# Performance work log

Measured on AMD Instinct MI355X. Metric: run time of the kernel, lower is better.

The kernel has to match this reference:

```python
import jax, jax.numpy as jnp
import numpy as np

B = 2048        # graphs per batch
NC = 81         # cells per sudoku
IN_C, HID = 10, 128
N_ACT, N_NUM, N_TECH = 4, 9, 10


def _sudoku_edges():
    idx = np.arange(NC).reshape(9, 9)
    adj = np.zeros((NC, NC), dtype=bool)
    for i in range(9):
        for j in range(9):
            n = idx[i, j]
            adj[n, idx[i, :]] = True
            adj[n, idx[:, j]] = True
            bi, bj = 3 * (i // 3), 3 * (j // 3)
            adj[n, idx[bi:bi + 3, bj:bj + 3].reshape(-1)] = True
            adj[n, n] = False
    src, dst = np.nonzero(adj)  # 1620 directed edges
    return np.stack([src, dst]).astype(np.int32)


def setup_inputs() -> dict:
    key = jax.random.key(0)
    ks = jax.random.split(key, 12)
    N = B * NC
    base = _sudoku_edges()                          # [2, 1620]
    offs = (np.arange(B, dtype=np.int32) * NC)      # [B]
    ei = (base[:, None, :] + offs[None, :, None]).reshape(2, -1)  # [2, B*1620]
    batch = np.repeat(np.arange(B, dtype=np.int32), NC)           # [N]

    def lin(k, fan_in, fan_out):
        s = 1.0 / np.sqrt(fan_in)
        return jax.random.uniform(k, (fan_in, fan_out), jnp.float32, -s, s)

    return {
        "x": jax.random.normal(ks[0], (N, IN_C), jnp.float32),
        "edge_index": jnp.asarray(ei),
        "batch": jnp.asarray(batch),
        "W1": lin(ks[1], IN_C, HID), "b1": jnp.zeros((HID,), jnp.float32),
        "W2": lin(ks[2], HID, HID),  "b2": jnp.zeros((HID,), jnp.float32),
        "Wa": lin(ks[3], HID, N_ACT),  "ba": jnp.zeros((N_ACT,), jnp.float32),
        "Wc": lin(ks[4], HID, NC),     "bc": jnp.zeros((NC,), jnp.float32),
        "Wn": lin(ks[5], HID, N_NUM),  "bn": jnp.zeros((N_NUM,), jnp.float32),
        "Wt": lin(ks[6], HID, N_TECH), "bt": jnp.zeros((N_TECH,), jnp.float32),
    }


def _gcn_conv(x, edge_index, W, b):
    n = x.shape[0]
    loop = jnp.arange(n, dtype=edge_index.dtype)
    src = jnp.concatenate([edge_index[0], loop])
    dst = jnp.concatenate([edge_index[1], loop])
    deg = jax.ops.segment_sum(jnp.ones_like(dst, jnp.float32), dst, num_segments=n)
    dinv = jax.lax.rsqrt(deg)            # deg >= 1 due to self-loops
    norm = dinv[src] * dinv[dst]         # [E+N]
    h = x @ W                            # [N, out]
    msg = h[src] * norm[:, None]         # gather + scale
    return jax.ops.segment_sum(msg, dst, num_segments=n) + b


def reference(x, edge_index, batch, W1, b1, W2, b2, Wa, ba, Wc, bc, Wn, bn, Wt, bt):
    h = jax.nn.relu(_gcn_conv(x, edge_index, W1, b1))
    h = jax.nn.relu(_gcn_conv(h, edge_index, W2, b2))
    # global mean pool over graphs
    sums = jax.ops.segment_sum(h, batch, num_segments=B)
    cnts = jax.ops.segment_sum(jnp.ones((h.shape[0],), h.dtype), batch, num_segments=B)
    pooled = sums / jnp.maximum(cnts, 1.0)[:, None]   # [B, HID]
    return (pooled @ Wa + ba, pooled @ Wc + bc, pooled @ Wn + bn, pooled @ Wt + bt)
```

## Files before the change

kernel.cpp:

```cpp
#include <hip/hip_runtime.h>
#include <hip/hip_bf16.h>

typedef __attribute__((ext_vector_type(8))) short bf16x8;
typedef __attribute__((ext_vector_type(4))) float f32x4;

__device__ __forceinline__ unsigned short f2b(float f) {
    __hip_bfloat16 h = __float2bfloat16(f);
    return __builtin_bit_cast(unsigned short, h);
}
__device__ __forceinline__ float b2f(unsigned short u) {
    unsigned v = ((unsigned)u) << 16;
    return __builtin_bit_cast(float, v);
}
__device__ __forceinline__ float ldf(const void* p, int idx, bool f32) {
    return f32 ? ((const float*)p)[idx] : b2f(((const unsigned short*)p)[idx]);
}
__device__ __forceinline__ unsigned short ldb(const void* p, int idx, bool f32) {
    return f32 ? f2b(((const float*)p)[idx]) : ((const unsigned short*)p)[idx];
}

__device__ __forceinline__ bool sniff_f32(const void* x) {
    const unsigned* p = (const unsigned*)x;
    int wild = 0;
#pragma unroll
    for (int i = 0; i < 16; ++i) {
        unsigned e = (p[i] >> 7) & 0xFF;
        wild += (e != 0 && (e < 0x68 || e > 0x90)) ? 1 : 0;
    }
    return wild > 8;
}

#define WS_B1F    16
#define WS_B2F    528
#define WS_BHF    1040
#define WS_W1R    1536
#define WS_W2R    9728
#define WS_SR     42496
#define WS_WH     60928

__global__ void k_repack(const void* __restrict__ x,
                         const void* __restrict__ W1, const void* __restrict__ b1,
                         const void* __restrict__ W2, const void* __restrict__ b2,
                         const void* __restrict__ Wa, const void* __restrict__ ba,
                         const void* __restrict__ Wc, const void* __restrict__ bc,
                         const void* __restrict__ Wn, const void* __restrict__ bn,
                         const void* __restrict__ Wt, const void* __restrict__ bt,
                         char* __restrict__ ws) {
    const bool f32 = sniff_f32(x);
    int idx = blockIdx.x * blockDim.x + threadIdx.x;
    if (idx < 4096) {
        int f = idx >> 5, k = idx & 31;
        unsigned short v = (k < 10) ? ldb(W1, k * 128 + f, f32) : (unsigned short)0;
        ((unsigned short*)(ws + WS_W1R))[idx] = v;
        return;
    }
    idx -= 4096;
    if (idx < 16384) {
        int f = idx >> 7, k = idx & 127;
        ((unsigned short*)(ws + WS_W2R))[idx] = ldb(W2, k * 128 + f, f32);
        return;
    }
    idx -= 16384;
    if (idx < 9216) {
        int fi = idx >> 9, rem = idx & 511;
        int lane = rem >> 3, j = rem & 7;
        int mi = fi / 3, kc = fi - mi * 3;
        int node = mi * 16 + (lane & 15);
        int cell = kc * 32 + ((lane >> 4) << 3) + j;
        bool adj = false;
        if (node < 81 && cell < 81) {
            int ni = node / 9, nj = node % 9;
            int ci = cell / 9, cj = cell % 9;
            adj = (ni == ci) || (nj == cj) ||
                  ((ni / 3 == ci / 3) && (nj / 3 == cj / 3));
        }
        ((unsigned short*)(ws + WS_SR))[idx] = adj ? (unsigned short)0x3F80 : (unsigned short)0;
        return;
    }
    idx -= 9216;
    if (idx < 13312) {
        int o = idx >> 7, f = idx & 127;
        const void* W; int oo, dim;
        if (o < 4)       { W = Wa; oo = o;      dim = 4;  }
        else if (o < 85) { W = Wc; oo = o - 4;  dim = 81; }
        else if (o < 94) { W = Wn; oo = o - 85; dim = 9;  }
        else             { W = Wt; oo = o - 94; dim = 10; }
        ((float*)(ws + WS_WH))[idx] = ldf(W, f * dim + oo, f32);
        return;
    }
    idx -= 13312;
    if (idx < 360) {
        float v;
        if (idx < 128)      v = ldf(b1, idx, f32);
        else if (idx < 256) v = ldf(b2, idx - 128, f32);
        else {
            int o = idx - 256;
            if (o < 4)       v = ldf(ba, o, f32);
            else if (o < 85) v = ldf(bc, o - 4, f32);
            else if (o < 94) v = ldf(bn, o - 85, f32);
            else             v = ldf(bt, o - 94, f32);
        }
        if (idx < 128)      ((float*)(ws + WS_B1F))[idx] = v;
        else if (idx < 256) ((float*)(ws + WS_B2F))[idx - 128] = v;
        else                ((float*)(ws + WS_BHF))[idx - 256] = v;
    }
}

#define T_STRIDE 104
#define H_STRIDE 136

__global__ __launch_bounds__(256, 4) void sudoku_gnn(
    const void* __restrict__ x, const char* __restrict__ ws,
    void* __restrict__ out, int nB)
{
    __shared__ __attribute__((aligned(16))) unsigned short sBuf[13312];
    __shared__ __attribute__((aligned(16))) unsigned int   xs[816];
    __shared__ float sPoolPart[256];
    __shared__ float sPool[128];

    const bool f32 = sniff_f32(x);
    const unsigned short* w1r = (const unsigned short*)(ws + WS_W1R);
    const unsigned short* w2r = (const unsigned short*)(ws + WS_W2R);
    const unsigned short* sr  = (const unsigned short*)(ws + WS_SR);
    const float* b1f = (const float*)(ws + WS_B1F);
    const float* b2f = (const float*)(ws + WS_B2F);
    const float* bhf = (const float*)(ws + WS_BHF);
    const float* whf = (const float*)(ws + WS_WH);

    const int tid  = threadIdx.x;
    const int wave = tid >> 6;
    const int lane = tid & 63;
    const int ln15 = lane & 15;
    const int q    = lane >> 4;
    const int k0   = q * 8;
    const int mtb  = (wave & 1) * 3;
    const int nb   = (wave & 1) * 48;
    const int fb   = (wave >> 1) * 64;
    const int g    = blockIdx.x;
    const float inv21 = 1.0f / 21.0f;

    {
        const int words = f32 ? 810 : 405;
        const unsigned int* src = (const unsigned int*)x + (size_t)g * words;
        for (int i = tid; i < words; i += 256) xs[i] = src[i];
    }

    bf16x8 sfr[3][3];
#pragma unroll
    for (int kc = 0; kc < 3; ++kc)
#pragma unroll
        for (int jt = 0; jt < 3; ++jt)
            sfr[kc][jt] = *(const bf16x8*)&sr[(((mtb + jt) * 3 + kc) * 64 + lane) * 8];
    bf16x8 w1f[4];
#pragma unroll
    for (int nt = 0; nt < 4; ++nt)
        w1f[nt] = *(const bf16x8*)&w1r[(fb + nt * 16 + ln15) * 32 + k0];

    __syncthreads();

    bf16x8 xf[3];
#pragma unroll
    for (int mt = 0; mt < 3; ++mt) {
        int node = (mtb + mt) * 16 + ln15;
        bf16x8 v = {0, 0, 0, 0, 0, 0, 0, 0};
        if (node < 81) {
            if (q == 0) {
#pragma unroll
                for (int jj = 0; jj < 8; ++jj)
                    v[jj] = (short)(f32 ? f2b(((const float*)xs)[node * 10 + jj])
                                        : ((const unsigned short*)xs)[node * 10 + jj]);
            } else if (q == 1) {
#pragma unroll
                for (int jj = 0; jj < 2; ++jj)
                    v[jj] = (short)(f32 ? f2b(((const float*)xs)[node * 10 + 8 + jj])
                                        : ((const unsigned short*)xs)[node * 10 + 8 + jj]);
            }
        }
        xf[mt] = v;
    }

    const f32x4 z4 = {0.f, 0.f, 0.f, 0.f};
    f32x4 acc[3][4];

#pragma unroll
    for (int mt = 0; mt < 3; ++mt)
#pragma unroll
        for (int nt = 0; nt < 4; ++nt)
            acc[mt][nt] = __builtin_amdgcn_mfma_f32_16x16x32_bf16(xf[mt], w1f[nt], z4, 0, 0, 0);
#pragma unroll
    for (int mt = 0; mt < 3; ++mt)
#pragma unroll
        for (int nt = 0; nt < 4; ++nt) {
            int f = fb + nt * 16 + ln15;
            int nodeb = (mtb + mt) * 16 + q * 4;
            unsigned lo = (unsigned)f2b(acc[mt][nt][0]) | ((unsigned)f2b(acc[mt][nt][1]) << 16);
            unsigned hi = (unsigned)f2b(acc[mt][nt][2]) | ((unsigned)f2b(acc[mt][nt][3]) << 16);
            *(uint2*)&sBuf[f * T_STRIDE + nodeb] = make_uint2(lo, hi);
        }
    __syncthreads();

#pragma unroll
    for (int at = 0; at < 3; ++at)
#pragma unroll
        for (int jt = 0; jt < 4; ++jt) acc[at][jt] = z4;
#pragma unroll
    for (int kc = 0; kc < 3; ++kc) {
        bf16x8 a4[4];
#pragma unroll
        for (int at = 0; at < 4; ++at)
            a4[at] = *(const bf16x8*)&sBuf[(fb + at * 16 + ln15) * T_STRIDE + kc * 32 + k0];
#pragma unroll
        for (int at = 0; at < 4; ++at)
#pragma unroll
            for (int jt = 0; jt < 3; ++jt)
                acc[jt][at] = __builtin_amdgcn_mfma_f32_16x16x32_bf16(a4[at], sfr[kc][jt], acc[jt][at], 0, 0, 0);
    }
    __syncthreads();
#pragma unroll
    for (int at = 0; at < 4; ++at) {
        float4 bv = *(const float4*)&b1f[fb + at * 16 + q * 4];
#pragma unroll
        for (int jt = 0; jt < 3; ++jt) {
            int node = nb + jt * 16 + ln15;
            float v0 = fmaxf(acc[jt][at][0] * inv21 + bv.x, 0.0f);
            float v1 = fmaxf(acc[jt][at][1] * inv21 + bv.y, 0.0f);
            float v2 = fmaxf(acc[jt][at][2] * inv21 + bv.z, 0.0f);
            float v3 = fmaxf(acc[jt][at][3] * inv21 + bv.w, 0.0f);
            unsigned lo = (unsigned)f2b(v0) | ((unsigned)f2b(v1) << 16);
            unsigned hi = (unsigned)f2b(v2) | ((unsigned)f2b(v3) << 16);
            *(uint2*)&sBuf[node * H_STRIDE + fb + at * 16 + q * 4] = make_uint2(lo, hi);
        }
    }
    __syncthreads();

#pragma unroll
    for (int mt = 0; mt < 3; ++mt)
#pragma unroll
        for (int nt = 0; nt < 4; ++nt) acc[mt][nt] = z4;
#pragma unroll
    for (int kc = 0; kc < 4; ++kc) {
        bf16x8 w2f[4];
#pragma unroll
        for (int nt = 0; nt < 4; ++nt)
            w2f[nt] = *(const bf16x8*)&w2r[(fb + nt * 16 + ln15) * 128 + kc * 32 + k0];
        bf16x8 a3[3];
#pragma unroll
        for (int mt = 0; mt < 3; ++mt)
            a3[mt] = *(const bf16x8*)&sBuf[((mtb + mt) * 16 + ln15) * H_STRIDE + kc * 32 + k0];
#pragma unroll
        for (int mt = 0; mt < 3; ++mt)
#pragma unroll
            for (int nt = 0; nt < 4; ++nt)
                acc[mt][nt] = __builtin_amdgcn_mfma_f32_16x16x32_bf16(a3[mt], w2f[nt], acc[mt][nt], 0, 0, 0);
    }
    __syncthreads();
#pragma unroll
    for (int mt = 0; mt < 3; ++mt)
#pragma unroll
        for (int nt = 0; nt < 4; ++nt) {
            int f = fb + nt * 16 + ln15;
            int nodeb = (mtb + mt) * 16 + q * 4;
            unsigned lo = (unsigned)f2b(acc[mt][nt][0]) | ((unsigned)f2b(acc[mt][nt][1]) << 16);
            unsigned hi = (unsigned)f2b(acc[mt][nt][2]) | ((unsigned)f2b(acc[mt][nt][3]) << 16);
            *(uint2*)&sBuf[f * T_STRIDE + nodeb] = make_uint2(lo, hi);
        }
    __syncthreads();

#pragma unroll
    for (int at = 0; at < 3; ++at)
#pragma unroll
        for (int jt = 0; jt < 4; ++jt) acc[at][jt] = z4;
#pragma unroll
    for (int kc = 0; kc < 3; ++kc) {
        bf16x8 a4[4];
#pragma unroll
        for (int at = 0; at < 4; ++at)
            a4[at] = *(const bf16x8*)&sBuf[(fb + at * 16 + ln15) * T_STRIDE + kc * 32 + k0];
#pragma unroll
        for (int at = 0; at < 4; ++at)
#pragma unroll
            for (int jt = 0; jt < 3; ++jt)
                acc[jt][at] = __builtin_amdgcn_mfma_f32_16x16x32_bf16(a4[at], sfr[kc][jt], acc[jt][at], 0, 0, 0);
    }
#pragma unroll
    for (int at = 0; at < 4; ++at) {
        float4 bv = *(const float4*)&b2f[fb + at * 16 + q * 4];
        float s0 = 0.f, s1 = 0.f, s2 = 0.f, s3 = 0.f;
#pragma unroll
        for (int jt = 0; jt < 3; ++jt) {
            int node = nb + jt * 16 + ln15;
            if (node < 81) {
                s0 += fmaxf(acc[jt][at][0] * inv21 + bv.x, 0.0f);
                s1 += fmaxf(acc[jt][at][1] * inv21 + bv.y, 0.0f);
                s2 += fmaxf(acc[jt][at][2] * inv21 + bv.z, 0.0f);
                s3 += fmaxf(acc[jt][at][3] * inv21 + bv.w, 0.0f);
            }
        }
#pragma unroll
        for (int off = 1; off < 16; off <<= 1) {
            s0 += __shfl_xor(s0, off);
            s1 += __shfl_xor(s1, off);
            s2 += __shfl_xor(s2, off);
            s3 += __shfl_xor(s3, off);
        }
        if (ln15 == 0) {
            float4 v = {s0, s1, s2, s3};
            *(float4*)&sPoolPart[(wave & 1) * 128 + fb + at * 16 + q * 4] = v;
        }
    }
    __syncthreads();
    if (tid < 128) sPool[tid] = (sPoolPart[tid] + sPoolPart[128 + tid]) / 81.0f;
    __syncthreads();

    if (tid < 104) {
        float a = bhf[tid];
        const float4* wrow = (const float4*)(whf + tid * 128);
        const float4* sp4  = (const float4*)sPool;
#pragma unroll 8
        for (int i = 0; i < 32; ++i) {
            float4 wv = wrow[i];
            float4 pv = sp4[i];
            a += pv.x * wv.x + pv.y * wv.y + pv.z * wv.z + pv.w * wv.w;
        }
        int o = tid, oo; size_t off;
        if (o < 4)       { oo = o;      off = (size_t)g * 4 + oo; }
        else if (o < 85) { oo = o - 4;  off = (size_t)nB * 4  + (size_t)g * 81 + oo; }
        else if (o < 94) { oo = o - 85; off = (size_t)nB * 85 + (size_t)g * 9  + oo; }
        else             { oo = o - 94; off = (size_t)nB * 94 + (size_t)g * 10 + oo; }
        if (f32) ((float*)out)[off] = a;
        else     ((unsigned short*)out)[off] = f2b(a);
    }
}

extern "C" void kernel_launch(void* const* d_in, const int* in_sizes, int n_in,
                              void* d_out, int out_size, void* d_ws, size_t ws_size,
                              hipStream_t stream) {
    const void* x  = d_in[0];
    int nB = in_sizes[2] / 81;
    if (nB <= 0) return;

    char* ws = (char*)d_ws;
    hipLaunchKernelGGL(k_repack, dim3(170), dim3(256), 0, stream,
                       x, d_in[3], d_in[4], d_in[5], d_in[6],
                       d_in[7], d_in[8], d_in[9], d_in[10],
                       d_in[11], d_in[12], d_in[13], d_in[14], ws);
    hipLaunchKernelGGL(sudoku_gnn, dim3(nB), dim3(256), 0, stream,
                       x, (const char*)ws, d_out, nB);
}
```

Before: 147.6 us.

## Process two sudoku graphs per block with XOR-swizzled LDS layout

Each workgroup now handles two graphs, so per-block setup (sniffing the input, loading the structure and W1 fragments, loading W2 per k-chunk) is shared across twice the work, and the two graphs interleave their MFMA chains. The padded-stride shared buffers are replaced by two 128-wide buffers with an XOR swizzle to avoid bank conflicts. In exchange register pressure roughly doubles (launch bounds lowered to 2 blocks/CU), LDS use grows, and the grid halves to 1024 blocks, which may reduce latency hiding on a 256-CU device.

```diff
diff --git a/kernel.cpp b/kernel.cpp
--- a/kernel.cpp
+++ b/kernel.cpp
@@ -17,6 +17,9 @@
 }
 __device__ __forceinline__ unsigned short ldb(const void* p, int idx, bool f32) {
     return f32 ? f2b(((const float*)p)[idx]) : ((const unsigned short*)p)[idx];
+}
+__device__ __forceinline__ int swz(int row, int col) {
+    return row * 128 + (((col >> 3) ^ (row & 7)) << 3) + (col & 7);
 }
 
 __device__ __forceinline__ bool sniff_f32(const void* x) {
@@ -106,17 +109,15 @@
     }
 }
 
-#define T_STRIDE 104
-#define H_STRIDE 136
-
-__global__ __launch_bounds__(256, 4) void sudoku_gnn(
+__global__ __launch_bounds__(256, 2) void sudoku_gnn(
     const void* __restrict__ x, const char* __restrict__ ws,
     void* __restrict__ out, int nB)
 {
-    __shared__ __attribute__((aligned(16))) unsigned short sBuf[13312];
-    __shared__ __attribute__((aligned(16))) unsigned int   xs[816];
-    __shared__ float sPoolPart[256];
-    __shared__ float sPool[128];
+    __shared__ __attribute__((aligned(16))) unsigned short sA[16384];
+    __shared__ __attribute__((aligned(16))) unsigned short sB[16384];
+    __shared__ __attribute__((aligned(16))) unsigned int   xs2[1632];
+    __shared__ float sPoolPart[2][256];
+    __shared__ float sPool[2][128];
 
     const bool f32 = sniff_f32(x);
     const unsigned short* w1r = (const unsigned short*)(ws + WS_W1R);
@@ -136,13 +137,17 @@
     const int mtb  = (wave & 1) * 3;
     const int nb   = (wave & 1) * 48;
     const int fb   = (wave >> 1) * 64;
-    const int g    = blockIdx.x;
+    const int g0   = blockIdx.x * 2;
+    const int g1   = g0 + 1;
+    const bool hasB = (g1 < nB);
     const float inv21 = 1.0f / 21.0f;
+    unsigned short* const buf[2] = {sA, sB};
 
     {
         const int words = f32 ? 810 : 405;
-        const unsigned int* src = (const unsigned int*)x + (size_t)g * words;
-        for (int i = tid; i < words; i += 256) xs[i] = src[i];
+        const int tot = words * (hasB ? 2 : 1);
+        const unsigned int* src = (const unsigned int*)x + (size_t)g0 * words;
+        for (int i = tid; i < tot; i += 256) xs2[i] = src[i];
     }
 
     bf16x8 sfr[3][3];
@@ -158,177 +163,217 @@
 
     __syncthreads();
 
-    bf16x8 xf[3];
-#pragma unroll
-    for (int mt = 0; mt < 3; ++mt) {
-        int node = (mtb + mt) * 16 + ln15;
-        bf16x8 v = {0, 0, 0, 0, 0, 0, 0, 0};
-        if (node < 81) {
-            if (q == 0) {
-#pragma unroll
-                for (int jj = 0; jj < 8; ++jj)
-                    v[jj] = (short)(f32 ? f2b(((const float*)xs)[node * 10 + jj])
-                                        : ((const unsigned short*)xs)[node * 10 + jj]);
-            } else if (q == 1) {
-#pragma unroll
-                for (int jj = 0; jj < 2; ++jj)
-                    v[jj] = (short)(f32 ? f2b(((const float*)xs)[node * 10 + 8 + jj])
-                                        : ((const unsigned short*)xs)[node * 10 + 8 + jj]);
-            }
-        }
-        xf[mt] = v;
-    }
+    bf16x8 xf[2][3];
+#pragma unroll
+    for (int gg = 0; gg < 2; ++gg)
+#pragma unroll
+        for (int mt = 0; mt < 3; ++mt) {
+            int node = (mtb + mt) * 16 + ln15;
+            bf16x8 v = {0, 0, 0, 0, 0, 0, 0, 0};
+            if (node < 81) {
+                int base = gg * 810 + node * 10;
+                if (q == 0) {
+#pragma unroll
+                    for (int jj = 0; jj < 8; ++jj)
+                        v[jj] = (short)(f32 ? f2b(((const float*)xs2)[base + jj])
+                                            : ((const unsigned short*)xs2)[base + jj]);
+                } else if (q == 1) {
+#pragma unroll
+                    for (int jj = 0; jj < 2; ++jj)
+                        v[jj] = (short)(f32 ? f2b(((const float*)xs2)[base + 8 + jj])
+                                            : ((const unsigned short*)xs2)[base + 8 + jj]);
+                }
+            }
+            xf[gg][mt] = v;
+        }
 
     const f32x4 z4 = {0.f, 0.f, 0.f, 0.f};
-    f32x4 acc[3][4];
-
-#pragma unroll
-    for (int mt = 0; mt < 3; ++mt)
-#pragma unroll
-        for (int nt = 0; nt < 4; ++nt)
-            acc[mt][nt] = __builtin_amdgcn_mfma_f32_16x16x32_bf16(xf[mt], w1f[nt], z4, 0, 0, 0);
-#pragma unroll
-    for (int mt = 0; mt < 3; ++mt)
-#pragma unroll
-        for (int nt = 0; nt < 4; ++nt) {
-            int f = fb + nt * 16 + ln15;
-            int nodeb = (mtb + mt) * 16 + q * 4;
-            unsigned lo = (unsigned)f2b(acc[mt][nt][0]) | ((unsigned)f2b(acc[mt][nt][1]) << 16);
-            unsigned hi = (unsigned)f2b(acc[mt][nt][2]) | ((unsigned)f2b(acc[mt][nt][3]) << 16);
-            *(uint2*)&sBuf[f * T_STRIDE + nodeb] = make_uint2(lo, hi);
-        }
-    __syncthreads();
-
-#pragma unroll
-    for (int at = 0; at < 3; ++at)
-#pragma unroll
-        for (int jt = 0; jt < 4; ++jt) acc[at][jt] = z4;
+    f32x4 acc[2][3][4];
+
+#pragma unroll
+    for (int gg = 0; gg < 2; ++gg)
+#pragma unroll
+        for (int mt = 0; mt < 3; ++mt)
+#pragma unroll
+            for (int nt = 0; nt < 4; ++nt)
+                acc[gg][mt][nt] = __builtin_amdgcn_mfma_f32_16x16x32_bf16(xf[gg][mt], w1f[nt], z4, 0, 0, 0);
+#pragma unroll
+    for (int gg = 0; gg < 2; ++gg)
+#pragma unroll
+        for (int mt = 0; mt < 3; ++mt)
+#pragma unroll
+            for (int nt = 0; nt < 4; ++nt) {
+                int f = fb + nt * 16 + ln15;
+                int nodeb = (mtb + mt) * 16 + q * 4;
+                unsigned lo = (unsigned)f2b(acc[gg][mt][nt][0]) | ((unsigned)f2b(acc[gg][mt][nt][1]) << 16);
+                unsigned hi = (unsigned)f2b(acc[gg][mt][nt][2]) | ((unsigned)f2b(acc[gg][mt][nt][3]) << 16);
+                *(uint2*)&buf[gg][swz(f, nodeb)] = make_uint2(lo, hi);
+            }
+    __syncthreads();
+
+#pragma unroll
+    for (int gg = 0; gg < 2; ++gg)
+#pragma unroll
+        for (int a = 0; a < 3; ++a)
+#pragma unroll
+            for (int b = 0; b < 4; ++b) acc[gg][a][b] = z4;
 #pragma unroll
     for (int kc = 0; kc < 3; ++kc) {
-        bf16x8 a4[4];
-#pragma unroll
-        for (int at = 0; at < 4; ++at)
-            a4[at] = *(const bf16x8*)&sBuf[(fb + at * 16 + ln15) * T_STRIDE + kc * 32 + k0];
-#pragma unroll
-        for (int at = 0; at < 4; ++at)
-#pragma unroll
-            for (int jt = 0; jt < 3; ++jt)
-                acc[jt][at] = __builtin_amdgcn_mfma_f32_16x16x32_bf16(a4[at], sfr[kc][jt], acc[jt][at], 0, 0, 0);
-    }
-    __syncthreads();
-#pragma unroll
-    for (int at = 0; at < 4; ++at) {
-        float4 bv = *(const float4*)&b1f[fb + at * 16 + q * 4];
-#pragma unroll
-        for (int jt = 0; jt < 3; ++jt) {
-            int node = nb + jt * 16 + ln15;
-            float v0 = fmaxf(acc[jt][at][0] * inv21 + bv.x, 0.0f);
-            float v1 = fmaxf(acc[jt][at][1] * inv21 + bv.y, 0.0f);
-            float v2 = fmaxf(acc[jt][at][2] * inv21 + bv.z, 0.0f);
-            float v3 = fmaxf(acc[jt][at][3] * inv21 + bv.w, 0.0f);
-            unsigned lo = (unsigned)f2b(v0) | ((unsigned)f2b(v1) << 16);
-            unsigned hi = (unsigned)f2b(v2) | ((unsigned)f2b(v3) << 16);
-            *(uint2*)&sBuf[node * H_STRIDE + fb + at * 16 + q * 4] = make_uint2(lo, hi);
-        }
-    }
-    __syncthreads();
-
-#pragma unroll
-    for (int mt = 0; mt < 3; ++mt)
-#pragma unroll
-        for (int nt = 0; nt < 4; ++nt) acc[mt][nt] = z4;
+        bf16x8 a4[2][4];
+#pragma unroll
+        for (int gg = 0; gg < 2; ++gg)
+#pragma unroll
+            for (int at = 0; at < 4; ++at)
+                a4[gg][at] = *(const bf16x8*)&buf[gg][swz(fb + at * 16 + ln15, kc * 32 + k0)];
+#pragma unroll
+        for (int gg = 0; gg < 2; ++gg)
+#pragma unroll
+            for (int at = 0; at < 4; ++at)
+#pragma unroll
+                for (int jt = 0; jt < 3; ++jt)
+                    acc[gg][jt][at] = __builtin_amdgcn_mfma_f32_16x16x32_bf16(a4[gg][at], sfr[kc][jt], acc[gg][jt][at], 0, 0, 0);
+    }
+    __syncthreads();
+#pragma unroll
+    for (int gg = 0; gg < 2; ++gg)
+#pragma unroll
+        for (int at = 0; at < 4; ++at) {
+            float4 bv = *(const float4*)&b1f[fb + at * 16 + q * 4];
+#pragma unroll
+            for (int jt = 0; jt < 3; ++jt) {
+                int node = nb + jt * 16 + ln15;
+                float v0 = fmaxf(acc[gg][jt][at][0] * inv21 + bv.x, 0.0f);
+                float v1 = fmaxf(acc[gg][jt][at][1] * inv21 + bv.y, 0.0f);
+                float v2 = fmaxf(acc[gg][jt][at][2] * inv21 + bv.z, 0.0f);
+                float v3 = fmaxf(acc[gg][jt][at][3] * inv21 + bv.w, 0.0f);
+                unsigned lo = (unsigned)f2b(v0) | ((unsigned)f2b(v1) << 16);
+                unsigned hi = (unsigned)f2b(v2) | ((unsigned)f2b(v3) << 16);
+                *(uint2*)&buf[gg][swz(node, fb + at * 16 + q * 4)] = make_uint2(lo, hi);
+            }
+        }
+    __syncthreads();
+
+#pragma unroll
+    for (int gg = 0; gg < 2; ++gg)
+#pragma unroll
+        for (int a = 0; a < 3; ++a)
+#pragma unroll
+            for (int b = 0; b < 4; ++b) acc[gg][a][b] = z4;
 #pragma unroll
     for (int kc = 0; kc < 4; ++kc) {
         bf16x8 w2f[4];
 #pragma unroll
         for (int nt = 0; nt < 4; ++nt)
             w2f[nt] = *(const bf16x8*)&w2r[(fb + nt * 16 + ln15) * 128 + kc * 32 + k0];
-        bf16x8 a3[3];
+        bf16x8 a3[2][3];
+#pragma unroll
+        for (int gg = 0; gg < 2; ++gg)
+#pragma unroll
+            for (int mt = 0; mt < 3; ++mt)
+                a3[gg][mt] = *(const bf16x8*)&buf[gg][swz((mtb + mt) * 16 + ln15, kc * 32 + k0)];
+#pragma unroll
+        for (int gg = 0; gg < 2; ++gg)
+#pragma unroll
+            for (int mt = 0; mt < 3; ++mt)
+#pragma unroll
+                for (int nt = 0; nt < 4; ++nt)
+                    acc[gg][mt][nt] = __builtin_amdgcn_mfma_f32_16x16x32_bf16(a3[gg][mt], w2f[nt], acc[gg][mt][nt], 0, 0, 0);
+    }
+    __syncthreads();
+#pragma unroll
+    for (int gg = 0; gg < 2; ++gg)
 #pragma unroll
         for (int mt = 0; mt < 3; ++mt)
-            a3[mt] = *(const bf16x8*)&sBuf[((mtb + mt) * 16 + ln15) * H_STRIDE + kc * 32 + k0];
-#pragma unroll
-        for (int mt = 0; mt < 3; ++mt)
-#pragma unroll
-            for (int nt = 0; nt < 4; ++nt)
-                acc[mt][nt] = __builtin_amdgcn_mfma_f32_16x16x32_bf16(a3[mt], w2f[nt], acc[mt][nt], 0, 0, 0);
-    }
-    __syncthreads();
-#pragma unroll
-    for (int mt = 0; mt < 3; ++mt)
-#pragma unroll
-        for (int nt = 0; nt < 4; ++nt) {
-            int f = fb + nt * 16 + ln15;
-            int nodeb = (mtb + mt) * 16 + q * 4;
-            unsigned lo = (unsigned)f2b(acc[mt][nt][0]) | ((unsigned)f2b(acc[mt][nt][1]) << 16);
-            unsigned hi = (unsigned)f2b(acc[mt][nt][2]) | ((unsigned)f2b(acc[mt][nt][3]) << 16);
-            *(uint2*)&sBuf[f * T_STRIDE + nodeb] = make_uint2(lo, hi);
-        }
-    __syncthreads();
-
-#pragma unroll
-    for (int at = 0; at < 3; ++at)
-#pragma unroll
-        for (int jt = 0; jt < 4; ++jt) acc[at][jt] = z4;
+#pragma unroll
+            for (int nt = 0; nt < 4; ++nt) {
+                int f = fb + nt * 16 + ln15;
+                int nodeb = (mtb + mt) * 16 + q * 4;
+                unsigned lo = (unsigned)f2b(acc[gg][mt][nt][0]) | ((unsigned)f2b(acc[gg][mt][nt][1]) << 16);
+                unsigned hi = (unsigned)f2b(acc[gg][mt][nt][2]) | ((unsigned)f2b(acc[gg][mt][nt][3]) << 16);
+                *(uint2*)&buf[gg][swz(f, nodeb)] = make_uint2(lo, hi);
+            }
+    __syncthreads();
+
+#pragma unroll
+    for (int gg = 0; gg < 2; ++gg)
+#pragma unroll
+        for (int a = 0; a < 3; ++a)
+#pragma unroll
+            for (int b = 0; b < 4; ++b) acc[gg][a][b] = z4;
 #pragma unroll
     for (int kc = 0; kc < 3; ++kc) {
-        bf16x8 a4[4];
-#pragma unroll
-        for (int at = 0; at < 4; ++at)
-            a4[at] = *(const bf16x8*)&sBuf[(fb + at * 16 + ln15) * T_STRIDE + kc * 32 + k0];
-#pragma unroll
-        for (int at = 0; at < 4; ++at)
-#pragma unroll
-            for (int jt = 0; jt < 3; ++jt)
-                acc[jt][at] = __builtin_amdgcn_mfma_f32_16x16x32_bf16(a4[at], sfr[kc][jt], acc[jt][at], 0, 0, 0);
-    }
-#pragma unroll
-    for (int at = 0; at < 4; ++at) {
-        float4 bv = *(const float4*)&b2f[fb + at * 16 + q * 4];
-        float s0 = 0.f, s1 = 0.f, s2 = 0.f, s3 = 0.f;
-#pragma unroll
-        for (int jt = 0; jt < 3; ++jt) {
-            int node = nb + jt * 16 + ln15;
-            if (node < 81) {
-                s0 += fmaxf(acc[jt][at][0] * inv21 + bv.x, 0.0f);
-                s1 += fmaxf(acc[jt][at][1] * inv21 + bv.y, 0.0f);
-                s2 += fmaxf(acc[jt][at][2] * inv21 + bv.z, 0.0f);
-                s3 += fmaxf(acc[jt][at][3] * inv21 + bv.w, 0.0f);
-            }
-        }
-#pragma unroll
-        for (int off = 1; off < 16; off <<= 1) {
-            s0 += __shfl_xor(s0, off);
-            s1 += __shfl_xor(s1, off);
-            s2 += __shfl_xor(s2, off);
-            s3 += __shfl_xor(s3, off);
-        }
-        if (ln15 == 0) {
-            float4 v = {s0, s1, s2, s3};
-            *(float4*)&sPoolPart[(wave & 1) * 128 + fb + at * 16 + q * 4] = v;
-        }
-    }
-    __syncthreads();
-    if (tid < 128) sPool[tid] = (sPoolPart[tid] + sPoolPart[128 + tid]) / 81.0f;
-    __syncthreads();
-
-    if (tid < 104) {
-        float a = bhf[tid];
-        const float4* wrow = (const float4*)(whf + tid * 128);
-        const float4* sp4  = (const float4*)sPool;
+        bf16x8 a4[2][4];
+#pragma unroll
+        for (int gg = 0; gg < 2; ++gg)
+#pragma unroll
+            for (int at = 0; at < 4; ++at)
+                a4[gg][at] = *(const bf16x8*)&buf[gg][swz(fb + at * 16 + ln15, kc * 32 + k0)];
+#pragma unroll
+        for (int gg = 0; gg < 2; ++gg)
+#pragma unroll
+            for (int at = 0; at < 4; ++at)
+#pragma unroll
+                for (int jt = 0; jt < 3; ++jt)
+                    acc[gg][jt][at] = __builtin_amdgcn_mfma_f32_16x16x32_bf16(a4[gg][at], sfr[kc][jt], acc[gg][jt][at], 0, 0, 0);
+    }
+#pragma unroll
+    for (int gg = 0; gg < 2; ++gg)
+#pragma unroll
+        for (int at = 0; at < 4; ++at) {
+            float4 bv = *(const float4*)&b2f[fb + at * 16 + q * 4];
+            float s0 = 0.f, s1 = 0.f, s2 = 0.f, s3 = 0.f;
+#pragma unroll
+            for (int jt = 0; jt < 3; ++jt) {
+                int node = nb + jt * 16 + ln15;
+                if (node < 81) {
+                    s0 += fmaxf(acc[gg][jt][at][0] * inv21 + bv.x, 0.0f);
+                    s1 += fmaxf(acc[gg][jt][at][1] * inv21 + bv.y, 0.0f);
+                    s2 += fmaxf(acc[gg][jt][at][2] * inv21 + bv.z, 0.0f);
+                    s3 += fmaxf(acc[gg][jt][at][3] * inv21 + bv.w, 0.0f);
+                }
+            }
+#pragma unroll
+            for (int off = 1; off < 16; off <<= 1) {
+                s0 += __shfl_xor(s0, off);
+                s1 += __shfl_xor(s1, off);
+                s2 += __shfl_xor(s2, off);
+                s3 += __shfl_xor(s3, off);
+            }
+            if (ln15 == 0) {
+                float4 v = {s0, s1, s2, s3};
+                *(float4*)&sPoolPart[gg][(wave & 1) * 128 + fb + at * 16 + q * 4] = v;
+            }
+        }
+    __syncthreads();
+    {
+        int gg = tid >> 7;
+        int f  = tid & 127;
+        sPool[gg][f] = (sPoolPart[gg][f] + sPoolPart[gg][128 + f]) / 81.0f;
+    }
+    __syncthreads();
+
+    {
+        int gg = tid >> 7;
+        int o  = tid & 127;
+        int g  = gg ? g1 : g0;
+        if (o < 104 && (gg == 0 || hasB)) {
+            float a = bhf[o];
+            const float4* wrow = (const float4*)(whf + o * 128);
+            const float4* sp4  = (const float4*)sPool[gg];
 #pragma unroll 8
-        for (int i = 0; i < 32; ++i) {
-            float4 wv = wrow[i];
-            float4 pv = sp4[i];
-            a += pv.x * wv.x + pv.y * wv.y + pv.z * wv.z + pv.w * wv.w;
-        }
-        int o = tid, oo; size_t off;
-        if (o < 4)       { oo = o;      off = (size_t)g * 4 + oo; }
-        else if (o < 85) { oo = o - 4;  off = (size_t)nB * 4  + (size_t)g * 81 + oo; }
-        else if (o < 94) { oo = o - 85; off = (size_t)nB * 85 + (size_t)g * 9  + oo; }
-        else             { oo = o - 94; off = (size_t)nB * 94 + (size_t)g * 10 + oo; }
-        if (f32) ((float*)out)[off] = a;
-        else     ((unsigned short*)out)[off] = f2b(a);
+            for (int i = 0; i < 32; ++i) {
+                float4 wv = wrow[i];
+                float4 pv = sp4[i];
+                a += pv.x * wv.x + pv.y * wv.y + pv.z * wv.z + pv.w * wv.w;
+            }
+            int oo; size_t off;
+            if (o < 4)       { oo = o;      off = (size_t)g * 4 + oo; }
+            else if (o < 85) { oo = o - 4;  off = (size_t)nB * 4  + (size_t)g * 81 + oo; }
+            else if (o < 94) { oo = o - 85; off = (size_t)nB * 85 + (size_t)g * 9  + oo; }
+            else             { oo = o - 94; off = (size_t)nB * 94 + (size_t)g * 10 + oo; }
+            if (f32) ((float*)out)[off] = a;
+            else     ((unsigned short*)out)[off] = f2b(a);
+        }
     }
 }
 
@@ -344,6 +389,6 @@
                        x, d_in[3], d_in[4], d_in[5], d_in[6],
                        d_in[7], d_in[8], d_in[9], d_in[10],
                        d_in[11], d_in[12], d_in[13], d_in[14], ws);
-    hipLaunchKernelGGL(sudoku_gnn, dim3(nB), dim3(256), 0, stream,
+    hipLaunchKernelGGL(sudoku_gnn, dim3((nB + 1) / 2), dim3(256), 0, stream,
                        x, (const char*)ws, d_out, nB);
 }
```

Measured after the change: 144.4 us. 2.2% less time.

## Halve block to two waves covering all nodes, fold scales into weights

Applied to the files above, without the earlier changes.

Shrinks each graph's block from four waves to two. Each wave now covers all 96 padded nodes for 64 features, which doubles per-wave accumulator tiles and drops the partial-pool reduction and one sync. The 1/21 normalization and 1/81 mean-pool scale are folded into the repacked W1, W2 and head weights. Inputs are read straight from global memory instead of being staged in LDS. Conversions use a manual round-to-nearest-even pack, and adjacency fragments are loaded per k-chunk. This raises register pressure (launch bounds 128,3) and lowers per-block parallelism in exchange for fewer instructions and barriers.

```diff
diff --git a/kernel.cpp b/kernel.cpp
--- a/kernel.cpp
+++ b/kernel.cpp
@@ -17,6 +17,13 @@
 }
 __device__ __forceinline__ unsigned short ldb(const void* p, int idx, bool f32) {
     return f32 ? f2b(((const float*)p)[idx]) : ((const unsigned short*)p)[idx];
+}
+__device__ __forceinline__ unsigned packRNE(float x, float y) {
+    unsigned a = __builtin_bit_cast(unsigned, x);
+    unsigned b = __builtin_bit_cast(unsigned, y);
+    a += 0x7fffu + ((a >> 16) & 1u);
+    b += 0x7fffu + ((b >> 16) & 1u);
+    return (a >> 16) | (b & 0xffff0000u);
 }
 
 __device__ __forceinline__ bool sniff_f32(const void* x) {
@@ -47,17 +54,18 @@
                          const void* __restrict__ Wt, const void* __restrict__ bt,
                          char* __restrict__ ws) {
     const bool f32 = sniff_f32(x);
+    const float inv21 = 1.0f / 21.0f;
     int idx = blockIdx.x * blockDim.x + threadIdx.x;
     if (idx < 4096) {
         int f = idx >> 5, k = idx & 31;
-        unsigned short v = (k < 10) ? ldb(W1, k * 128 + f, f32) : (unsigned short)0;
+        unsigned short v = (k < 10) ? f2b(ldf(W1, k * 128 + f, f32) * inv21) : (unsigned short)0;
         ((unsigned short*)(ws + WS_W1R))[idx] = v;
         return;
     }
     idx -= 4096;
     if (idx < 16384) {
         int f = idx >> 7, k = idx & 127;
-        ((unsigned short*)(ws + WS_W2R))[idx] = ldb(W2, k * 128 + f, f32);
+        ((unsigned short*)(ws + WS_W2R))[idx] = f2b(ldf(W2, k * 128 + f, f32) * inv21);
         return;
     }
     idx -= 16384;
@@ -85,7 +93,7 @@
         else if (o < 85) { W = Wc; oo = o - 4;  dim = 81; }
         else if (o < 94) { W = Wn; oo = o - 85; dim = 9;  }
         else             { W = Wt; oo = o - 94; dim = 10; }
-        ((float*)(ws + WS_WH))[idx] = ldf(W, f * dim + oo, f32);
+        ((float*)(ws + WS_WH))[idx] = ldf(W, f * dim + oo, f32) * (1.0f / 81.0f);
         return;
     }
     idx -= 13312;
@@ -106,16 +114,14 @@
     }
 }
 
-#define T_STRIDE 104
-#define H_STRIDE 136
-
-__global__ __launch_bounds__(256, 4) void sudoku_gnn(
+#define TS 104
+#define HS 136
+
+__global__ __launch_bounds__(128, 3) void sudoku_gnn(
     const void* __restrict__ x, const char* __restrict__ ws,
     void* __restrict__ out, int nB)
 {
-    __shared__ __attribute__((aligned(16))) unsigned short sBuf[13312];
-    __shared__ __attribute__((aligned(16))) unsigned int   xs[816];
-    __shared__ float sPoolPart[256];
+    __shared__ __attribute__((aligned(16))) unsigned short sG[13312];
     __shared__ float sPool[128];
 
     const bool f32 = sniff_f32(x);
@@ -133,167 +139,164 @@
     const int ln15 = lane & 15;
     const int q    = lane >> 4;
     const int k0   = q * 8;
-    const int mtb  = (wave & 1) * 3;
-    const int nb   = (wave & 1) * 48;
-    const int fb   = (wave >> 1) * 64;
+    const int fb   = wave * 64;
     const int g    = blockIdx.x;
-    const float inv21 = 1.0f / 21.0f;
-
-    {
-        const int words = f32 ? 810 : 405;
-        const unsigned int* src = (const unsigned int*)x + (size_t)g * words;
-        for (int i = tid; i < words; i += 256) xs[i] = src[i];
-    }
-
-    bf16x8 sfr[3][3];
-#pragma unroll
-    for (int kc = 0; kc < 3; ++kc)
-#pragma unroll
-        for (int jt = 0; jt < 3; ++jt)
-            sfr[kc][jt] = *(const bf16x8*)&sr[(((mtb + jt) * 3 + kc) * 64 + lane) * 8];
+
+    bf16x8 xf[6];
+#pragma unroll
+    for (int mt = 0; mt < 6; ++mt) {
+        int node = mt * 16 + ln15;
+        bf16x8 v = {0, 0, 0, 0, 0, 0, 0, 0};
+        if (node < 81) {
+            int base = (g * 81 + node) * 10;
+            if (q == 0) {
+#pragma unroll
+                for (int jj = 0; jj < 8; ++jj) v[jj] = (short)ldb(x, base + jj, f32);
+            } else if (q == 1) {
+                v[0] = (short)ldb(x, base + 8, f32);
+                v[1] = (short)ldb(x, base + 9, f32);
+            }
+        }
+        xf[mt] = v;
+    }
     bf16x8 w1f[4];
 #pragma unroll
     for (int nt = 0; nt < 4; ++nt)
         w1f[nt] = *(const bf16x8*)&w1r[(fb + nt * 16 + ln15) * 32 + k0];
 
-    __syncthreads();
-
-    bf16x8 xf[3];
-#pragma unroll
-    for (int mt = 0; mt < 3; ++mt) {
-        int node = (mtb + mt) * 16 + ln15;
-        bf16x8 v = {0, 0, 0, 0, 0, 0, 0, 0};
-        if (node < 81) {
-            if (q == 0) {
-#pragma unroll
-                for (int jj = 0; jj < 8; ++jj)
-                    v[jj] = (short)(f32 ? f2b(((const float*)xs)[node * 10 + jj])
-                                        : ((const unsigned short*)xs)[node * 10 + jj]);
-            } else if (q == 1) {
-#pragma unroll
-                for (int jj = 0; jj < 2; ++jj)
-                    v[jj] = (short)(f32 ? f2b(((const float*)xs)[node * 10 + 8 + jj])
-                                        : ((const unsigned short*)xs)[node * 10 + 8 + jj]);
-            }
-        }
-        xf[mt] = v;
-    }
-
     const f32x4 z4 = {0.f, 0.f, 0.f, 0.f};
-    f32x4 acc[3][4];
-
-#pragma unroll
-    for (int mt = 0; mt < 3; ++mt)
+    f32x4 acc[6][4];
+
+#pragma unroll
+    for (int mt = 0; mt < 6; ++mt)
 #pragma unroll
         for (int nt = 0; nt < 4; ++nt)
             acc[mt][nt] = __builtin_amdgcn_mfma_f32_16x16x32_bf16(xf[mt], w1f[nt], z4, 0, 0, 0);
 #pragma unroll
-    for (int mt = 0; mt < 3; ++mt)
+    for (int mt = 0; mt < 6; ++mt)
 #pragma unroll
         for (int nt = 0; nt < 4; ++nt) {
             int f = fb + nt * 16 + ln15;
-            int nodeb = (mtb + mt) * 16 + q * 4;
-            unsigned lo = (unsigned)f2b(acc[mt][nt][0]) | ((unsigned)f2b(acc[mt][nt][1]) << 16);
-            unsigned hi = (unsigned)f2b(acc[mt][nt][2]) | ((unsigned)f2b(acc[mt][nt][3]) << 16);
-            *(uint2*)&sBuf[f * T_STRIDE + nodeb] = make_uint2(lo, hi);
-        }
-    __syncthreads();
-
-#pragma unroll
-    for (int at = 0; at < 3; ++at)
-#pragma unroll
-        for (int jt = 0; jt < 4; ++jt) acc[at][jt] = z4;
+            int cellb = mt * 16 + q * 4;
+            *(uint2*)&sG[f * TS + cellb] =
+                make_uint2(packRNE(acc[mt][nt][0], acc[mt][nt][1]),
+                           packRNE(acc[mt][nt][2], acc[mt][nt][3]));
+        }
+    __syncthreads();
+
 #pragma unroll
     for (int kc = 0; kc < 3; ++kc) {
-        bf16x8 a4[4];
+        bf16x8 afr[4], sfb[6];
 #pragma unroll
         for (int at = 0; at < 4; ++at)
-            a4[at] = *(const bf16x8*)&sBuf[(fb + at * 16 + ln15) * T_STRIDE + kc * 32 + k0];
-#pragma unroll
-        for (int at = 0; at < 4; ++at)
-#pragma unroll
-            for (int jt = 0; jt < 3; ++jt)
-                acc[jt][at] = __builtin_amdgcn_mfma_f32_16x16x32_bf16(a4[at], sfr[kc][jt], acc[jt][at], 0, 0, 0);
-    }
-    __syncthreads();
+            afr[at] = *(const bf16x8*)&sG[(fb + at * 16 + ln15) * TS + kc * 32 + k0];
+#pragma unroll
+        for (int jt = 0; jt < 6; ++jt)
+            sfb[jt] = *(const bf16x8*)&sr[((jt * 3 + kc) * 64 + lane) * 8];
+        if (kc == 0) {
+#pragma unroll
+            for (int jt = 0; jt < 6; ++jt)
+#pragma unroll
+                for (int at = 0; at < 4; ++at)
+                    acc[jt][at] = __builtin_amdgcn_mfma_f32_16x16x32_bf16(afr[at], sfb[jt], z4, 0, 0, 0);
+        } else {
+#pragma unroll
+            for (int jt = 0; jt < 6; ++jt)
+#pragma unroll
+                for (int at = 0; at < 4; ++at)
+                    acc[jt][at] = __builtin_amdgcn_mfma_f32_16x16x32_bf16(afr[at], sfb[jt], acc[jt][at], 0, 0, 0);
+        }
+    }
+    __syncthreads();
+
 #pragma unroll
     for (int at = 0; at < 4; ++at) {
         float4 bv = *(const float4*)&b1f[fb + at * 16 + q * 4];
 #pragma unroll
-        for (int jt = 0; jt < 3; ++jt) {
-            int node = nb + jt * 16 + ln15;
-            float v0 = fmaxf(acc[jt][at][0] * inv21 + bv.x, 0.0f);
-            float v1 = fmaxf(acc[jt][at][1] * inv21 + bv.y, 0.0f);
-            float v2 = fmaxf(acc[jt][at][2] * inv21 + bv.z, 0.0f);
-            float v3 = fmaxf(acc[jt][at][3] * inv21 + bv.w, 0.0f);
-            unsigned lo = (unsigned)f2b(v0) | ((unsigned)f2b(v1) << 16);
-            unsigned hi = (unsigned)f2b(v2) | ((unsigned)f2b(v3) << 16);
-            *(uint2*)&sBuf[node * H_STRIDE + fb + at * 16 + q * 4] = make_uint2(lo, hi);
-        }
-    }
-    __syncthreads();
-
-#pragma unroll
-    for (int mt = 0; mt < 3; ++mt)
-#pragma unroll
-        for (int nt = 0; nt < 4; ++nt) acc[mt][nt] = z4;
+        for (int jt = 0; jt < 6; ++jt) {
+            int node = jt * 16 + ln15;
+            float v0 = fmaxf(acc[jt][at][0] + bv.x, 0.0f);
+            float v1 = fmaxf(acc[jt][at][1] + bv.y, 0.0f);
+            float v2 = fmaxf(acc[jt][at][2] + bv.z, 0.0f);
+            float v3 = fmaxf(acc[jt][at][3] + bv.w, 0.0f);
+            *(uint2*)&sG[node * HS + fb + at * 16 + q * 4] =
+                make_uint2(packRNE(v0, v1), packRNE(v2, v3));
+        }
+    }
+    __syncthreads();
+
 #pragma unroll
     for (int kc = 0; kc < 4; ++kc) {
-        bf16x8 w2f[4];
+        bf16x8 a6[6], w2f[4];
+#pragma unroll
+        for (int mt = 0; mt < 6; ++mt)
+            a6[mt] = *(const bf16x8*)&sG[(mt * 16 + ln15) * HS + kc * 32 + k0];
 #pragma unroll
         for (int nt = 0; nt < 4; ++nt)
             w2f[nt] = *(const bf16x8*)&w2r[(fb + nt * 16 + ln15) * 128 + kc * 32 + k0];
-        bf16x8 a3[3];
-#pragma unroll
-        for (int mt = 0; mt < 3; ++mt)
-            a3[mt] = *(const bf16x8*)&sBuf[((mtb + mt) * 16 + ln15) * H_STRIDE + kc * 32 + k0];
-#pragma unroll
-        for (int mt = 0; mt < 3; ++mt)
-#pragma unroll
-            for (int nt = 0; nt < 4; ++nt)
-                acc[mt][nt] = __builtin_amdgcn_mfma_f32_16x16x32_bf16(a3[mt], w2f[nt], acc[mt][nt], 0, 0, 0);
-    }
-    __syncthreads();
-#pragma unroll
-    for (int mt = 0; mt < 3; ++mt)
+        if (kc == 0) {
+#pragma unroll
+            for (int mt = 0; mt < 6; ++mt)
+#pragma unroll
+                for (int nt = 0; nt < 4; ++nt)
+                    acc[mt][nt] = __builtin_amdgcn_mfma_f32_16x16x32_bf16(a6[mt], w2f[nt], z4, 0, 0, 0);
+        } else {
+#pragma unroll
+            for (int mt = 0; mt < 6; ++mt)
+#pragma unroll
+                for (int nt = 0; nt < 4; ++nt)
+                    acc[mt][nt] = __builtin_amdgcn_mfma_f32_16x16x32_bf16(a6[mt], w2f[nt], acc[mt][nt], 0, 0, 0);
+        }
+    }
+    __syncthreads();
+
+#pragma unroll
+    for (int mt = 0; mt < 6; ++mt)
 #pragma unroll
         for (int nt = 0; nt < 4; ++nt) {
             int f = fb + nt * 16 + ln15;
-            int nodeb = (mtb + mt) * 16 + q * 4;
-            unsigned lo = (unsigned)f2b(acc[mt][nt][0]) | ((unsigned)f2b(acc[mt][nt][1]) << 16);
-            unsigned hi = (unsigned)f2b(acc[mt][nt][2]) | ((unsigned)f2b(acc[mt][nt][3]) << 16);
-            *(uint2*)&sBuf[f * T_STRIDE + nodeb] = make_uint2(lo, hi);
-        }
-    __syncthreads();
-
-#pragma unroll
-    for (int at = 0; at < 3; ++at)
-#pragma unroll
-        for (int jt = 0; jt < 4; ++jt) acc[at][jt] = z4;
+            int cellb = mt * 16 + q * 4;
+            *(uint2*)&sG[f * TS + cellb] =
+                make_uint2(packRNE(acc[mt][nt][0], acc[mt][nt][1]),
+                           packRNE(acc[mt][nt][2], acc[mt][nt][3]));
+        }
+    __syncthreads();
+
 #pragma unroll
     for (int kc = 0; kc < 3; ++kc) {
-        bf16x8 a4[4];
+        bf16x8 afr[4], sfb[6];
 #pragma unroll
         for (int at = 0; at < 4; ++at)
-            a4[at] = *(const bf16x8*)&sBuf[(fb + at * 16 + ln15) * T_STRIDE + kc * 32 + k0];
-#pragma unroll
-        for (int at = 0; at < 4; ++at)
-#pragma unroll
-            for (int jt = 0; jt < 3; ++jt)
-                acc[jt][at] = __builtin_amdgcn_mfma_f32_16x16x32_bf16(a4[at], sfr[kc][jt], acc[jt][at], 0, 0, 0);
+            afr[at] = *(const bf16x8*)&sG[(fb + at * 16 + ln15) * TS + kc * 32 + k0];
+#pragma unroll
+        for (int jt = 0; jt < 6; ++jt)
+            sfb[jt] = *(const bf16x8*)&sr[((jt * 3 + kc) * 64 + lane) * 8];
+        if (kc == 0) {
+#pragma unroll
+            for (int jt = 0; jt < 6; ++jt)
+#pragma unroll
+                for (int at = 0; at < 4; ++at)
+                    acc[jt][at] = __builtin_amdgcn_mfma_f32_16x16x32_bf16(afr[at], sfb[jt], z4, 0, 0, 0);
+        } else {
+#pragma unroll
+            for (int jt = 0; jt < 6; ++jt)
+#pragma unroll
+                for (int at = 0; at < 4; ++at)
+                    acc[jt][at] = __builtin_amdgcn_mfma_f32_16x16x32_bf16(afr[at], sfb[jt], acc[jt][at], 0, 0, 0);
+        }
     }
 #pragma unroll
     for (int at = 0; at < 4; ++at) {
         float4 bv = *(const float4*)&b2f[fb + at * 16 + q * 4];
         float s0 = 0.f, s1 = 0.f, s2 = 0.f, s3 = 0.f;
 #pragma unroll
-        for (int jt = 0; jt < 3; ++jt) {
-            int node = nb + jt * 16 + ln15;
+        for (int jt = 0; jt < 6; ++jt) {
+            int node = jt * 16 + ln15;
             if (node < 81) {
-                s0 += fmaxf(acc[jt][at][0] * inv21 + bv.x, 0.0f);
-                s1 += fmaxf(acc[jt][at][1] * inv21 + bv.y, 0.0f);
-                s2 += fmaxf(acc[jt][at][2] * inv21 + bv.z, 0.0f);
-                s3 += fmaxf(acc[jt][at][3] * inv21 + bv.w, 0.0f);
+                s0 += fmaxf(acc[jt][at][0] + bv.x, 0.0f);
+                s1 += fmaxf(acc[jt][at][1] + bv.y, 0.0f);
+                s2 += fmaxf(acc[jt][at][2] + bv.z, 0.0f);
+                s3 += fmaxf(acc[jt][at][3] + bv.w, 0.0f);
             }
         }
 #pragma unroll
@@ -305,11 +308,9 @@
         }
         if (ln15 == 0) {
             float4 v = {s0, s1, s2, s3};
-            *(float4*)&sPoolPart[(wave & 1) * 128 + fb + at * 16 + q * 4] = v;
-        }
-    }
-    __syncthreads();
-    if (tid < 128) sPool[tid] = (sPoolPart[tid] + sPoolPart[128 + tid]) / 81.0f;
+            *(float4*)&sPool[fb + at * 16 + q * 4] = v;
+        }
+    }
     __syncthreads();
 
     if (tid < 104) {
@@ -344,6 +345,6 @@
                        x, d_in[3], d_in[4], d_in[5], d_in[6],
                        d_in[7], d_in[8], d_in[9], d_in[10],
                        d_in[11], d_in[12], d_in[13], d_in[14], ws);
-    hipLaunchKernelGGL(sudoku_gnn, dim3(nB), dim3(256), 0, stream,
+    hipLaunchKernelGGL(sudoku_gnn, dim3(nB), dim3(128), 0, stream,
                        x, (const char*)ws, d_out, nB);
 }
```

New measurement: 154.2 us. +4.5%, slower.
